# Kernel optimization log

Measured on AMD Instinct MI355X. Metric: run time of the kernel, lower is better.

Reference implementation:

```python
import jax, jax.numpy as jnp
import numpy as np

KSIZE = 7
NSPIX = 196


def _unfold(x, k):
    # x: (T, C, H, W) -> (T, C, k*k, H, W), reflect padding, torch Unfold ordering
    p = (k - 1) // 2
    T, C, H, W = x.shape
    xp = jnp.pad(x, ((0, 0), (0, 0), (p, p), (p, p)), mode='reflect')
    return jnp.stack([xp[:, :, i:i + H, j:j + W] for i in range(k) for j in range(k)], axis=2)


def setup_inputs() -> dict:
    key = jax.random.key(0)
    k1, k2, k3, k4, k5 = jax.random.split(key, 5)
    T, C, H, W = 2, 64, 160, 160
    fan_in = C * KSIZE * KSIZE
    x = jax.random.normal(k1, (T, C, H, W), jnp.float32)
    spix = jax.random.randint(k2, (T, H, W), 0, NSPIX, jnp.int32)
    W_lin = jax.random.normal(k3, (C, fan_in), jnp.float32) / np.sqrt(fan_in)
    b_lin = jax.random.normal(k4, (C,), jnp.float32) * 0.01
    w_scale = jax.random.normal(k5, (C,), jnp.float32) / np.sqrt(C)
    b_scale = jnp.zeros((1,), jnp.float32)
    return {"x": x, "spix": spix, "W_lin": W_lin, "b_lin": b_lin,
            "w_scale": w_scale, "b_scale": b_scale}


def reference(x, spix, W_lin, b_lin, w_scale, b_scale):
    T, C, H, W = x.shape
    K2 = KSIZE * KSIZE
    O = W_lin.shape[0]
    p = (KSIZE - 1) // 2

    # unfold(x) with reflect padding -> patches (T, C, K2, H, W)
    patches = _unfold(x, KSIZE)

    # unfold(spix) -> neighbor superpixel ids per pixel (T, K2, H, W)
    sp = jnp.pad(spix, ((0, 0), (p, p), (p, p)), mode='reflect')
    nb = jnp.stack([sp[:, i:i + H, j:j + W] for i in range(KSIZE) for j in range(KSIZE)], axis=1)

    # per-frame superpixel mean pooling (bist.get_pooled_video): down (T, S, C)
    seg = (spix.astype(jnp.int32) + jnp.arange(T, dtype=jnp.int32)[:, None, None] * NSPIX).reshape(-1)
    feats = x.transpose(0, 2, 3, 1).reshape(-1, C)  # (T*H*W, C)
    sums = jax.ops.segment_sum(feats, seg, num_segments=T * NSPIX).reshape(T, NSPIX, C)
    cnts = jax.ops.segment_sum(jnp.ones((seg.shape[0],), x.dtype), seg,
                               num_segments=T * NSPIX).reshape(T, NSPIX, 1)
    down = sums / jnp.maximum(cnts, 1.0)

    # squared pairwise distances between superpixel means: pwd (T, S, S)
    sq = jnp.sum(down * down, axis=-1)
    pwd = jnp.maximum(sq[:, :, None] + sq[:, None, :]
                      - 2.0 * jnp.einsum('tsc,tuc->tsu', down, down), 0.0)

    # sims[t,k,h,w] = ||mean(spix[t,h,w]) - mean(nb[t,k,h,w])||^2
    tidx = jnp.arange(T)[:, None, None, None]
    sims = pwd[tidx, spix[:, None, :, :], nb]  # (T, K2, H, W)

    # scale = 10 * softplus(1x1-conv(x / ||x||_c))  -> (T, H, W)
    xn = x / (jnp.linalg.norm(x, axis=1, keepdims=True) + 1e-10)
    scale = 10.0 * jax.nn.softplus(jnp.einsum('c,tchw->thw', w_scale, xn) + b_scale[0])

    # apply_norm 'exp_max' over the kernel-tap axis
    rw = jnp.exp(-scale[:, None, :, :] * sims)  # (T, K2, H, W)
    rw = rw / (1e-5 + jnp.max(rw, axis=1, keepdims=True))

    # dynamic conv: out[t,o,h,w] = sum_{c,k} W[o,c,k] * patches[t,c,k,h,w] * rw[t,k,h,w] + b[o]
    out = jnp.einsum('ock,tckhw,tkhw->tohw', W_lin.reshape(O, C, K2), patches, rw)
    return out + b_lin[None, :, None, None]
```

## Files before the change

kernel.cpp:

```cpp
#include <hip/hip_runtime.h>
#include <math.h>

#define TT 2
#define CC 64
#define HH 160
#define WW 160
#define KS 7
#define K2 49
#define NSPIX 196
#define HWSZ (HH*WW)
#define PAD 3
#define OO 64
#define FANIN (CC*K2)
#define TS 8
#define PS (TS+KS-1)
#define NPOS (PS*PS)

#define NCHUNK 25
#define CHUNKPIX 1024

typedef _Float16 half8 __attribute__((ext_vector_type(8)));
typedef float f32x16 __attribute__((ext_vector_type(16)));
typedef unsigned int uint4v __attribute__((ext_vector_type(4)));
typedef _Float16 half2v __attribute__((ext_vector_type(2)));

__device__ __forceinline__ int reflect(int i, int n) {
    if (i < 0) i = -i;
    if (i >= n) i = 2*n - 2 - i;
    return i;
}

__global__ __launch_bounds__(256) void k_prep(const float* __restrict__ x,
                                              const int* __restrict__ spix,
                                              const float* __restrict__ Wl,
                                              const float* __restrict__ wsc,
                                              const float* __restrict__ bsc,
                                              float* __restrict__ sums,
                                              float* __restrict__ cnts,
                                              float* __restrict__ scale,
                                              _Float16* __restrict__ Wb,
                                              _Float16* __restrict__ xT) {
    __shared__ float ls[4*200];
    __shared__ float lcnt[200];
    int bid = blockIdx.x;
    int tid = threadIdx.x;

    if (bid < 800) {
        int cg = bid & 15;
        int rest = bid >> 4;
        int ch = rest % NCHUNK;
        int t  = rest / NCHUNK;

        for (int i = tid; i < 4*200; i += 256) ls[i] = 0.f;
        if (cg == 0) for (int i = tid; i < 200; i += 256) lcnt[i] = 0.f;
        __syncthreads();

        int base = ch*CHUNKPIX;
        const int4* sp4 = (const int4*)(spix + t*HWSZ + base);
        int4 sv = sp4[tid];
        if (cg == 0) {
            atomicAdd(&lcnt[sv.x], 1.f); atomicAdd(&lcnt[sv.y], 1.f);
            atomicAdd(&lcnt[sv.z], 1.f); atomicAdd(&lcnt[sv.w], 1.f);
        }
        const float* xb = x + ((size_t)t*CC + cg*4)*HWSZ + base;
        #pragma unroll
        for (int j = 0; j < 4; ++j) {
            float4 xv = *(const float4*)(xb + (size_t)j*HWSZ + tid*4);
            float* lj = &ls[j*200];
            atomicAdd(&lj[sv.x], xv.x);
            atomicAdd(&lj[sv.y], xv.y);
            atomicAdd(&lj[sv.z], xv.z);
            atomicAdd(&lj[sv.w], xv.w);
        }
        __syncthreads();

        float* sb = sums + (size_t)t*NSPIX*CC + cg*4;
        for (int i = tid; i < 4*NSPIX; i += 256) {
            int s = i >> 2, j = i & 3;
            float v = ls[j*200 + s];
            if (v != 0.f) atomicAdd(&sb[s*CC + j], v);
        }
        if (cg == 0)
            for (int i = tid; i < NSPIX; i += 256) {
                float v = lcnt[i];
                if (v != 0.f) atomicAdd(&cnts[t*NSPIX + i], v);
            }
    } else if (bid < 1000) {
        int pix = (bid - 800)*256 + tid;
        int t = pix / HWSZ, hw = pix - t*HWSZ;
        const float* xs = x + (size_t)t*CC*HWSZ + hw;
        float s1 = 0.f, s2 = 0.f;
        unsigned int pk[32];
        #pragma unroll
        for (int cp = 0; cp < 32; ++cp) {
            float v0 = xs[(size_t)(2*cp)*HWSZ];
            float v1 = xs[(size_t)(2*cp + 1)*HWSZ];
            s1 += wsc[2*cp]*v0 + wsc[2*cp+1]*v1;
            s2 = fmaf(v0, v0, s2); s2 = fmaf(v1, v1, s2);
            half2v h; h[0] = (_Float16)v0; h[1] = (_Float16)v1;
            pk[cp] = __builtin_bit_cast(unsigned int, h);
        }
        float z = s1/(sqrtf(s2) + 1e-10f) + bsc[0];
        float sp_ = (z > 0.f) ? z + log1pf(expf(-z)) : log1pf(expf(z));
        scale[pix] = 10.f*sp_;
        uint4v* dst = (uint4v*)(xT + (size_t)pix*64);
        #pragma unroll
        for (int q = 0; q < 8; ++q) {
            uint4v v = { pk[4*q], pk[4*q+1], pk[4*q+2], pk[4*q+3] };
            dst[q] = v;
        }
    } else {
        int row = (bid - 1000)*256 + tid;
        if (row < 2*K2*4*64) {
            int ln  = row & 63;
            int kc  = (row >> 6) & 3;
            int tq  = row >> 8;
            int tap = tq % K2;
            int qo  = tq / K2;
            int o = qo*32 + (ln & 31);
            int cb = kc*16 + (ln >> 5)*8;
            _Float16* dst = Wb + (size_t)row*8;
            const float* src = Wl + (size_t)o*FANIN + tap;
            #pragma unroll
            for (int j = 0; j < 8; ++j) dst[j] = (_Float16)src[(size_t)(cb + j)*K2];
        }
    }
}

__global__ __launch_bounds__(256) void k_pwd(const float* __restrict__ sums,
                                             const float* __restrict__ cnts,
                                             float* __restrict__ pwd) {
    int tid = blockIdx.x*256 + threadIdx.x;
    if (tid >= TT*NSPIX*NSPIX) return;
    int t = tid / (NSPIX*NSPIX); int r = tid - t*NSPIX*NSPIX;
    int s = r / NSPIX, u = r - (r / NSPIX)*NSPIX;
    const float4* ds4 = (const float4*)(sums + (size_t)(t*NSPIX + s)*CC);
    const float4* du4 = (const float4*)(sums + (size_t)(t*NSPIX + u)*CC);
    float is = 1.0f / fmaxf(cnts[t*NSPIX + s], 1.0f);
    float iu = 1.0f / fmaxf(cnts[t*NSPIX + u], 1.0f);
    float acc = 0.f;
    #pragma unroll
    for (int q = 0; q < 16; ++q) {
        float4 a = ds4[q], b = du4[q];
        float d0 = a.x*is - b.x*iu;
        float d1 = a.y*is - b.y*iu;
        float d2 = a.z*is - b.z*iu;
        float d3 = a.w*is - b.w*iu;
        acc = fmaf(d0, d0, acc);
        acc = fmaf(d1, d1, acc);
        acc = fmaf(d2, d2, acc);
        acc = fmaf(d3, d3, acc);
    }
    pwd[tid] = acc;
}

__global__ __launch_bounds__(256, 4) void k_main(
    const _Float16* __restrict__ xT, const int* __restrict__ spix,
    const _Float16* __restrict__ Wb, const float* __restrict__ b_lin,
    const float* __restrict__ pwd, const float* __restrict__ scale,
    float* __restrict__ out)
{
    __shared__ unsigned short xpT[NPOS*64];
    __shared__ unsigned short rwb[K2*64];
    __shared__ int   sp[NPOS];
    __shared__ float mxp[4*64];

    int bid0 = blockIdx.x;
    int bid = (bid0 & 7)*100 + (bid0 >> 3);
    int t = bid / 400;
    int r = bid - t*400;
    int th0 = (r / 20)*TS, tw0 = (r - (r/20)*20)*TS;
    int tid = threadIdx.y*64 + threadIdx.x;

    for (int i = tid; i < NPOS; i += 256) {
        int rr = reflect(th0 + i/PS - PAD, HH);
        int cc = reflect(tw0 + i%PS - PAD, WW);
        sp[i] = spix[t*HWSZ + rr*WW + cc];
    }
    {
        const _Float16* xt = xT + (size_t)t*HWSZ*64;
        for (int i = tid; i < NPOS*8; i += 256) {
            int pos = i >> 3, cb = i & 7;
            int rr = reflect(th0 + pos/PS - PAD, HH);
            int cc = reflect(tw0 + pos%PS - PAD, WW);
            uint4v v = *(const uint4v*)(xt + (size_t)(rr*WW + cc)*64 + cb*8);
            int chunk = cb ^ (pos & 7);
            *(uint4v*)&xpT[pos*64 + chunk*8] = v;
        }
    }
    __syncthreads();

    int p_ = threadIdx.x;
    int ty = threadIdx.y;
    int py0 = p_ >> 3, px0 = p_ & 7;
    {
        float sc = scale[t*HWSZ + (th0 + py0)*WW + (tw0 + px0)];
        int s0 = sp[(py0 + PAD)*PS + (px0 + PAD)];
        const float* pr = pwd + (t*NSPIX + s0)*NSPIX;
        float pmax = 0.f;
        for (int k = ty; k < K2; k += 4) {
            int di = k/KS, dj = k - di*KS;
            int nb = sp[(py0 + di)*PS + (px0 + dj)];
            float v = __expf(-sc * pr[nb]);
            rwb[k*64 + p_] = __builtin_bit_cast(unsigned short, (_Float16)v);
            pmax = fmaxf(pmax, v);
        }
        mxp[ty*64 + p_] = pmax;
    }
    __syncthreads();

    int ln = threadIdx.x;
    int wv = __builtin_amdgcn_readfirstlane(threadIdx.y);
    int qp = wv & 1, kh = wv >> 1;
    int p  = qp*32 + (ln & 31);
    int ppy = p >> 3, ppx = p & 7;
    int lhi = ln >> 5;

    int jc0 = 4*kh + lhi, jc1 = jc0 + 2;

    const _Float16* A0b = Wb + (size_t)(2*kh)*512 + ln*8;
    const _Float16* A1b = A0b + (size_t)K2*4*512;

    f32x16 acc0, acc1;
    #pragma unroll
    for (int i = 0; i < 16; ++i) { acc0[i] = 0.f; acc1[i] = 0.f; }

    int di = 0, dj = 0;
    #pragma unroll 7
    for (int tap = 0; tap < K2; ++tap) {
        const _Float16* a0 = A0b + (size_t)tap*2048;
        half8 A00 = *(const half8*)(a0);
        half8 A01 = *(const half8*)(a0 + 512);
        const _Float16* a1 = A1b + (size_t)tap*2048;
        half8 A10 = *(const half8*)(a1);
        half8 A11 = *(const half8*)(a1 + 512);

        int pos = (ppy + di)*PS + (ppx + dj);
        int sw  = pos & 7;
        const unsigned short* bbase = &xpT[pos*64];
        half8 B0 = *(const half8*)(bbase + ((jc0 ^ sw) << 3));
        half8 B1 = *(const half8*)(bbase + ((jc1 ^ sw) << 3));

        _Float16 rh = __builtin_bit_cast(_Float16, rwb[tap*64 + p]);
        half8 rv8 = { rh, rh, rh, rh, rh, rh, rh, rh };
        half8 b0 = B0 * rv8;
        half8 b1 = B1 * rv8;

        acc0 = __builtin_amdgcn_mfma_f32_32x32x16_f16(A00, b0, acc0, 0, 0, 0);
        acc1 = __builtin_amdgcn_mfma_f32_32x32x16_f16(A10, b0, acc1, 0, 0, 0);
        acc0 = __builtin_amdgcn_mfma_f32_32x32x16_f16(A01, b1, acc0, 0, 0, 0);
        acc1 = __builtin_amdgcn_mfma_f32_32x32x16_f16(A11, b1, acc1, 0, 0, 0);

        if (++dj == KS) { dj = 0; ++di; }
    }

    __syncthreads();
    float* red = (float*)xpT;
    if (kh == 1) {
        #pragma unroll
        for (int i = 0; i < 16; ++i) {
            red[((qp*2 + 0)*16 + i)*64 + ln] = acc0[i];
            red[((qp*2 + 1)*16 + i)*64 + ln] = acc1[i];
        }
    }
    __syncthreads();
    if (kh == 0) {
        float m = fmaxf(fmaxf(mxp[p], mxp[64 + p]), fmaxf(mxp[128 + p], mxp[192 + p]));
        float s = 1.f/(1e-5f + m);
        int h = th0 + ppy, w = tw0 + ppx;
        int row_hi = 4*lhi;
        float* ob = out + (size_t)t*OO*HWSZ + h*WW + w;
        #pragma unroll
        for (int rg = 0; rg < 16; ++rg) {
            int o0 = (rg & 3) + 8*(rg >> 2) + row_hi;
            int o1 = 32 + o0;
            float v0 = acc0[rg] + red[((qp*2 + 0)*16 + rg)*64 + ln];
            float v1 = acc1[rg] + red[((qp*2 + 1)*16 + rg)*64 + ln];
            ob[(size_t)o0*HWSZ] = v0*s + b_lin[o0];
            ob[(size_t)o1*HWSZ] = v1*s + b_lin[o1];
        }
    }
}

extern "C" void kernel_launch(void* const* d_in, const int* in_sizes, int n_in,
                              void* d_out, int out_size, void* d_ws, size_t ws_size,
                              hipStream_t stream) {
    const float* x    = (const float*)d_in[0];
    const int*   spix = (const int*)d_in[1];
    const float* Wl   = (const float*)d_in[2];
    const float* bl   = (const float*)d_in[3];
    const float* wsc  = (const float*)d_in[4];
    const float* bsc  = (const float*)d_in[5];
    float* out = (float*)d_out;

    float* ws    = (float*)d_ws;
    float* sums  = ws;
    float* cnts  = sums + TT*NSPIX*CC;
    float* pwd   = cnts + TT*NSPIX;
    float* scale = pwd  + TT*NSPIX*NSPIX;
    _Float16* Wb = (_Float16*)(scale + TT*HWSZ);
    _Float16* xT = Wb + (size_t)2*K2*4*64*8;

    hipMemsetAsync(sums, 0, (size_t)(TT*NSPIX*CC + TT*NSPIX)*sizeof(float), stream);

    k_prep<<<1098, 256, 0, stream>>>(x, spix, Wl, wsc, bsc, sums, cnts, scale, Wb, xT);
    k_pwd <<<(TT*NSPIX*NSPIX + 255)/256, 256, 0, stream>>>(sums, cnts, pwd);

    dim3 blk(64, 4, 1);
    k_main<<<TT*400, blk, 0, stream>>>(xT, spix, Wb, bl, pwd, scale, out);
}
```

Measured before the change: 149.0 us.

## Split tap loop across two wave groups with 512-thread blocks and staged reduction

```diff
diff --git a/kernel.cpp b/kernel.cpp
--- a/kernel.cpp
+++ b/kernel.cpp
@@ -154,7 +154,7 @@
     pwd[tid] = acc;
 }
 
-__global__ __launch_bounds__(256, 4) void k_main(
+__global__ __launch_bounds__(512, 8) void k_main(
     const _Float16* __restrict__ xT, const int* __restrict__ spix,
     const _Float16* __restrict__ Wb, const float* __restrict__ b_lin,
     const float* __restrict__ pwd, const float* __restrict__ scale,
@@ -163,7 +163,7 @@
     __shared__ unsigned short xpT[NPOS*64];
     __shared__ unsigned short rwb[K2*64];
     __shared__ int   sp[NPOS];
-    __shared__ float mxp[4*64];
+    __shared__ float mxp[8*64];
 
     int bid0 = blockIdx.x;
     int bid = (bid0 & 7)*100 + (bid0 >> 3);
@@ -172,14 +172,14 @@
     int th0 = (r / 20)*TS, tw0 = (r - (r/20)*20)*TS;
     int tid = threadIdx.y*64 + threadIdx.x;
 
-    for (int i = tid; i < NPOS; i += 256) {
+    for (int i = tid; i < NPOS; i += 512) {
         int rr = reflect(th0 + i/PS - PAD, HH);
         int cc = reflect(tw0 + i%PS - PAD, WW);
         sp[i] = spix[t*HWSZ + rr*WW + cc];
     }
     {
         const _Float16* xt = xT + (size_t)t*HWSZ*64;
-        for (int i = tid; i < NPOS*8; i += 256) {
+        for (int i = tid; i < NPOS*8; i += 512) {
             int pos = i >> 3, cb = i & 7;
             int rr = reflect(th0 + pos/PS - PAD, HH);
             int cc = reflect(tw0 + pos%PS - PAD, WW);
@@ -198,7 +198,7 @@
         int s0 = sp[(py0 + PAD)*PS + (px0 + PAD)];
         const float* pr = pwd + (t*NSPIX + s0)*NSPIX;
         float pmax = 0.f;
-        for (int k = ty; k < K2; k += 4) {
+        for (int k = ty; k < K2; k += 8) {
             int di = k/KS, dj = k - di*KS;
             int nb = sp[(py0 + di)*PS + (px0 + dj)];
             float v = __expf(-sc * pr[nb]);
@@ -211,7 +211,7 @@
 
     int ln = threadIdx.x;
     int wv = __builtin_amdgcn_readfirstlane(threadIdx.y);
-    int qp = wv & 1, kh = wv >> 1;
+    int qp = wv & 1, kh = (wv >> 1) & 1, tg = wv >> 2;
     int p  = qp*32 + (ln & 31);
     int ppy = p >> 3, ppx = p & 7;
     int lhi = ln >> 5;
@@ -225,9 +225,11 @@
     #pragma unroll
     for (int i = 0; i < 16; ++i) { acc0[i] = 0.f; acc1[i] = 0.f; }
 
-    int di = 0, dj = 0;
-    #pragma unroll 7
-    for (int tap = 0; tap < K2; ++tap) {
+    int tap0 = tg ? 25 : 0;
+    int tap1 = tg ? K2 : 25;
+    int di = tg ? 3 : 0, dj = tg ? 4 : 0;
+    #pragma unroll 5
+    for (int tap = tap0; tap < tap1; ++tap) {
         const _Float16* a0 = A0b + (size_t)tap*2048;
         half8 A00 = *(const half8*)(a0);
         half8 A01 = *(const half8*)(a0 + 512);
@@ -256,16 +258,27 @@
 
     __syncthreads();
     float* red = (float*)xpT;
-    if (kh == 1) {
-        #pragma unroll
-        for (int i = 0; i < 16; ++i) {
-            red[((qp*2 + 0)*16 + i)*64 + ln] = acc0[i];
-            red[((qp*2 + 1)*16 + i)*64 + ln] = acc1[i];
-        }
-    }
-    __syncthreads();
-    if (kh == 0) {
-        float m = fmaxf(fmaxf(mxp[p], mxp[64 + p]), fmaxf(mxp[128 + p], mxp[192 + p]));
+    #define RED_W  { _Pragma("unroll") for (int i = 0; i < 16; ++i) { \
+            red[((qp*2 + 0)*16 + i)*64 + ln] = acc0[i]; \
+            red[((qp*2 + 1)*16 + i)*64 + ln] = acc1[i]; } }
+    #define RED_R  { _Pragma("unroll") for (int i = 0; i < 16; ++i) { \
+            acc0[i] += red[((qp*2 + 0)*16 + i)*64 + ln]; \
+            acc1[i] += red[((qp*2 + 1)*16 + i)*64 + ln]; } }
+    if (tg == 1 && kh == 0) RED_W
+    __syncthreads();
+    if (tg == 0 && kh == 0) RED_R
+    __syncthreads();
+    if (tg == 1 && kh == 1) RED_W
+    __syncthreads();
+    if (tg == 0 && kh == 1) RED_R
+    __syncthreads();
+    if (tg == 0 && kh == 1) RED_W
+    __syncthreads();
+    if (tg == 0 && kh == 0) {
+        RED_R
+        float m = mxp[p];
+        #pragma unroll
+        for (int q = 1; q < 8; ++q) m = fmaxf(m, mxp[q*64 + p]);
         float s = 1.f/(1e-5f + m);
         int h = th0 + ppy, w = tw0 + ppx;
         int row_hi = 4*lhi;
@@ -274,12 +287,12 @@
         for (int rg = 0; rg < 16; ++rg) {
             int o0 = (rg & 3) + 8*(rg >> 2) + row_hi;
             int o1 = 32 + o0;
-            float v0 = acc0[rg] + red[((qp*2 + 0)*16 + rg)*64 + ln];
-            float v1 = acc1[rg] + red[((qp*2 + 1)*16 + rg)*64 + ln];
-            ob[(size_t)o0*HWSZ] = v0*s + b_lin[o0];
-            ob[(size_t)o1*HWSZ] = v1*s + b_lin[o1];
-        }
-    }
+            ob[(size_t)o0*HWSZ] = acc0[rg]*s + b_lin[o0];
+            ob[(size_t)o1*HWSZ] = acc1[rg]*s + b_lin[o1];
+        }
+    }
+    #undef RED_W
+    #undef RED_R
 }
 
 extern "C" void kernel_launch(void* const* d_in, const int* in_sizes, int n_in,
@@ -306,6 +319,6 @@
     k_prep<<<1098, 256, 0, stream>>>(x, spix, Wl, wsc, bsc, sums, cnts, scale, Wb, xT);
     k_pwd <<<(TT*NSPIX*NSPIX + 255)/256, 256, 0, stream>>>(sums, cnts, pwd);
 
-    dim3 blk(64, 4, 1);
+    dim3 blk(64, 8, 1);
     k_main<<<TT*400, blk, 0, stream>>>(xT, spix, Wb, bl, pwd, scale, out);
 }
```

Result: slower. 152.7 us (+2.5%).
